# Kernel tuning notes

Measured on AMD Instinct MI355X. Metric: run time of the kernel, lower is better.

## Reference

```python
import jax, jax.numpy as jnp
from jax import lax
import numpy as np

B, T, IN, H, L = 4096, 1024, 2, 16, 3


def _lstm_layer(x_tbd, h0, c0, Wih, Whh, b):
    # x_tbd: [T, B, D_in]; returns hidden states [T, B, H]
    def step(carry, xt):
        h, c = carry
        g = xt @ Wih.T + h @ Whh.T + b  # [B, 4H], gate order i,f,g,o (PyTorch)
        i, f, gg, o = jnp.split(g, 4, axis=-1)
        i = jax.nn.sigmoid(i)
        f = jax.nn.sigmoid(f)
        gg = jnp.tanh(gg)
        o = jax.nn.sigmoid(o)
        c = f * c + i * gg
        h = o * jnp.tanh(c)
        return (h, c), h

    _, hs = lax.scan(step, (h0, c0), x_tbd)
    return hs


def setup_inputs() -> dict:
    key = jax.random.key(0)
    ks = jax.random.split(key, 16)

    def xavier(k, shape):
        fan_out, fan_in = shape
        s = jnp.sqrt(6.0 / (fan_in + fan_out)).astype(jnp.float32)
        return jax.random.uniform(k, shape, jnp.float32, -1.0, 1.0) * s

    inp = {
        "x": jax.random.normal(ks[0], (B, T, IN), jnp.float32),
        "h0": jax.random.normal(ks[1], (L, B, H), jnp.float32) * 0.1,
        "c0": jax.random.normal(ks[2], (L, B, H), jnp.float32) * 0.1,
        "W_ih0": xavier(ks[3], (4 * H, IN)),
        "W_hh0": xavier(ks[4], (4 * H, H)),
        "b_ih0": jnp.zeros((4 * H,), jnp.float32),
        "b_hh0": jnp.zeros((4 * H,), jnp.float32),
        "W_ih1": xavier(ks[5], (4 * H, H)),
        "W_hh1": xavier(ks[6], (4 * H, H)),
        "b_ih1": jnp.zeros((4 * H,), jnp.float32),
        "b_hh1": jnp.zeros((4 * H,), jnp.float32),
        "W_ih2": xavier(ks[7], (4 * H, H)),
        "W_hh2": xavier(ks[8], (4 * H, H)),
        "b_ih2": jnp.zeros((4 * H,), jnp.float32),
        "b_hh2": jnp.zeros((4 * H,), jnp.float32),
        "W_fc": xavier(ks[9], (1, H)),
        "b_fc": jnp.zeros((1,), jnp.float32),
    }
    return inp


def reference(x, h0, c0, W_ih0, W_hh0, b_ih0, b_hh0, W_ih1, W_hh1, b_ih1, b_hh1,
              W_ih2, W_hh2, b_ih2, b_hh2, W_fc, b_fc):
    layers = [
        (W_ih0, W_hh0, b_ih0 + b_hh0),
        (W_ih1, W_hh1, b_ih1 + b_hh1),
        (W_ih2, W_hh2, b_ih2 + b_hh2),
    ]
    h = jnp.transpose(x, (1, 0, 2))  # [T, B, IN]
    for l, (Wih, Whh, b) in enumerate(layers):
        h = _lstm_layer(h, h0[l], c0[l], Wih, Whh, b)  # [T, B, H]
    last = h[-1]  # [B, H] == out[:, -1, :]
    return last @ W_fc.T + b_fc  # [B, 1]
```

## Files before the change

### kernel.cpp

```cpp
#include <hip/hip_runtime.h>

#define NB 4096
#define NT 1024

typedef float f2 __attribute__((ext_vector_type(2)));
typedef float f4 __attribute__((ext_vector_type(4)));

#define GATE(accv, creg, hout) {                                              \
    float e_ = __builtin_amdgcn_exp2f((accv) * kpre);                         \
    float r_ = __builtin_amdgcn_rcpf(1.0f + e_);                              \
    float a_ = fmaf(r_, kA, kB);                                              \
    int ai_ = __float_as_int(a_);                                             \
    float iv_ = __int_as_float(__builtin_amdgcn_mov_dpp(ai_, 0x00, 0xF, 0xF, 0)); \
    float fv_ = __int_as_float(__builtin_amdgcn_mov_dpp(ai_, 0x55, 0xF, 0xF, 0)); \
    float gv_ = __int_as_float(__builtin_amdgcn_mov_dpp(ai_, 0xAA, 0xF, 0xF, 0)); \
    float ov_ = __int_as_float(__builtin_amdgcn_mov_dpp(ai_, 0xFF, 0xF, 0xF, 0)); \
    creg = fmaf(fv_, creg, iv_ * gv_);                                        \
    float e2_ = __builtin_amdgcn_exp2f(creg * -2.88539008177792681f);         \
    float r2_ = __builtin_amdgcn_rcpf(1.0f + e2_);                            \
    hout = ov_ * fmaf(r2_, 2.0f, -1.0f);                                      \
}

__global__ __launch_bounds__(256, 4) void lstm3_kernel(
    const float* __restrict__ x,
    const float* __restrict__ h0,
    const float* __restrict__ c0,
    const float* __restrict__ Wih0, const float* __restrict__ Whh0,
    const float* __restrict__ bih0, const float* __restrict__ bhh0,
    const float* __restrict__ Wih1, const float* __restrict__ Whh1,
    const float* __restrict__ bih1, const float* __restrict__ bhh1,
    const float* __restrict__ Wih2, const float* __restrict__ Whh2,
    const float* __restrict__ bih2, const float* __restrict__ bhh2,
    const float* __restrict__ Wfc,  const float* __restrict__ bfc,
    float* __restrict__ out)
{
    __shared__ float ldsH[3][4][16];
    __shared__ float ldsX[4][64];

    const int lane = threadIdx.x & 63;
    const int wv   = threadIdx.x >> 6;
    const int b    = (blockIdx.x << 2) + wv;
    const int q    = lane >> 2;
    const int g    = lane & 3;
    const int row  = g * 16 + q;

    const float kpre = (g == 2) ? -2.88539008177792681f : -1.44269504088896340f;
    const float kA   = (g == 2) ? 2.0f : 1.0f;
    const float kB   = (g == 2) ? -1.0f : 0.0f;

    f2 wi0 = *(const f2*)&Wih0[row * 2];
    f4 wh0[4], wi1[4], wh1[4], wi2[4], wh2[4];
#pragma unroll
    for (int k = 0; k < 4; ++k) {
        wh0[k] = *(const f4*)&Whh0[row * 16 + 4 * k];
        wi1[k] = *(const f4*)&Wih1[row * 16 + 4 * k];
        wh1[k] = *(const f4*)&Whh1[row * 16 + 4 * k];
        wi2[k] = *(const f4*)&Wih2[row * 16 + 4 * k];
        wh2[k] = *(const f4*)&Whh2[row * 16 + 4 * k];
    }
    float bias0 = bih0[row] + bhh0[row];
    float bias1 = bih1[row] + bhh1[row];
    float bias2 = bih2[row] + bhh2[row];
    asm volatile("" : "+v"(wh0[0]), "+v"(wh0[1]), "+v"(wh0[2]), "+v"(wh0[3]));
    asm volatile("" : "+v"(wi1[0]), "+v"(wi1[1]), "+v"(wi1[2]), "+v"(wi1[3]));
    asm volatile("" : "+v"(wh1[0]), "+v"(wh1[1]), "+v"(wh1[2]), "+v"(wh1[3]));
    asm volatile("" : "+v"(wi2[0]), "+v"(wi2[1]), "+v"(wi2[2]), "+v"(wi2[3]));
    asm volatile("" : "+v"(wh2[0]), "+v"(wh2[1]), "+v"(wh2[2]), "+v"(wh2[3]));
    asm volatile("" : "+v"(wi0), "+v"(bias0), "+v"(bias1), "+v"(bias2));

    float c0r = c0[0 * NB * 16 + b * 16 + q];
    float c1r = c0[1 * NB * 16 + b * 16 + q];
    float c2r = c0[2 * NB * 16 + b * 16 + q];
    if (lane < 16) {
        ldsH[0][wv][lane] = h0[0 * NB * 16 + b * 16 + lane];
        ldsH[1][wv][lane] = h0[1 * NB * 16 + b * 16 + lane];
        ldsH[2][wv][lane] = h0[2 * NB * 16 + b * 16 + lane];
    }
    __builtin_amdgcn_wave_barrier();

    const f4* __restrict__ hb0 = (const f4*)&ldsH[0][wv][0];
    const f4* __restrict__ hb1 = (const f4*)&ldsH[1][wv][0];
    const f4* __restrict__ hb2 = (const f4*)&ldsH[2][wv][0];
    const f2* __restrict__ xb  = (const f2*)&ldsX[wv][0];

    float xpre = x[(size_t)b * (NT * 2) + lane];

    for (int ch = 0; ch < (NT * 2) / 64; ++ch) {
        ldsX[wv][lane] = xpre;
        __builtin_amdgcn_wave_barrier();
        if (ch + 1 < (NT * 2) / 64)
            xpre = x[(size_t)b * (NT * 2) + (ch + 1) * 64 + lane];

#pragma unroll 2
        for (int s = 0; s < 32; ++s) {
            const f2 x2 = xb[s];

            f4 ha = hb0[0], hc = hb0[1], hd = hb0[2], he = hb0[3];
            f4 a0 = wh0[0] * ha;
            f4 a1 = wh0[1] * hc;
            a0 = wh0[2] * hd + a0;
            a1 = wh0[3] * he + a1;
            a0 = a0 + a1;
            f2 s2 = __builtin_shufflevector(a0, a0, 0, 1)
                  + __builtin_shufflevector(a0, a0, 2, 3);
            float acc = (s2.x + s2.y) + fmaf(wi0.x, x2.x, fmaf(wi0.y, x2.y, bias0));
            float hn0;
            GATE(acc, c0r, hn0);
            if (g == 0) ldsH[0][wv][q] = hn0;
            __builtin_amdgcn_wave_barrier();

            ha = hb1[0]; hc = hb1[1]; hd = hb1[2]; he = hb1[3];
            f4 xa = hb0[0], xc = hb0[1], xd = hb0[2], xe = hb0[3];
            a0 = wh1[0] * ha;
            a1 = wh1[1] * hc;
            f4 a2 = wh1[2] * hd;
            f4 a3 = wh1[3] * he;
            a0 = wi1[0] * xa + a0;
            a1 = wi1[1] * xc + a1;
            a2 = wi1[2] * xd + a2;
            a3 = wi1[3] * xe + a3;
            a0 = a0 + a1;
            a2 = a2 + a3;
            a0 = a0 + a2;
            s2 = __builtin_shufflevector(a0, a0, 0, 1)
               + __builtin_shufflevector(a0, a0, 2, 3);
            acc = (s2.x + s2.y) + bias1;
            float hn1;
            GATE(acc, c1r, hn1);
            if (g == 0) ldsH[1][wv][q] = hn1;
            __builtin_amdgcn_wave_barrier();

            ha = hb2[0]; hc = hb2[1]; hd = hb2[2]; he = hb2[3];
            xa = hb1[0]; xc = hb1[1]; xd = hb1[2]; xe = hb1[3];
            a0 = wh2[0] * ha;
            a1 = wh2[1] * hc;
            a2 = wh2[2] * hd;
            a3 = wh2[3] * he;
            a0 = wi2[0] * xa + a0;
            a1 = wi2[1] * xc + a1;
            a2 = wi2[2] * xd + a2;
            a3 = wi2[3] * xe + a3;
            a0 = a0 + a1;
            a2 = a2 + a3;
            a0 = a0 + a2;
            s2 = __builtin_shufflevector(a0, a0, 0, 1)
               + __builtin_shufflevector(a0, a0, 2, 3);
            acc = (s2.x + s2.y) + bias2;
            float hn2;
            GATE(acc, c2r, hn2);
            if (g == 0) ldsH[2][wv][q] = hn2;
            __builtin_amdgcn_wave_barrier();
        }
    }

    if (lane == 0) {
        float s = bfc[0];
#pragma unroll
        for (int k = 0; k < 16; ++k) s = fmaf(ldsH[2][wv][k], Wfc[k], s);
        out[b] = s;
    }
}

extern "C" void kernel_launch(void* const* d_in, const int* in_sizes, int n_in,
                              void* d_out, int out_size, void* d_ws, size_t ws_size,
                              hipStream_t stream) {
    (void)in_sizes; (void)n_in; (void)d_ws; (void)ws_size; (void)out_size;
    const float* x    = (const float*)d_in[0];
    const float* h0   = (const float*)d_in[1];
    const float* c0   = (const float*)d_in[2];
    const float* Wih0 = (const float*)d_in[3];
    const float* Whh0 = (const float*)d_in[4];
    const float* bih0 = (const float*)d_in[5];
    const float* bhh0 = (const float*)d_in[6];
    const float* Wih1 = (const float*)d_in[7];
    const float* Whh1 = (const float*)d_in[8];
    const float* bih1 = (const float*)d_in[9];
    const float* bhh1 = (const float*)d_in[10];
    const float* Wih2 = (const float*)d_in[11];
    const float* Whh2 = (const float*)d_in[12];
    const float* bih2 = (const float*)d_in[13];
    const float* bhh2 = (const float*)d_in[14];
    const float* Wfc  = (const float*)d_in[15];
    const float* bfc  = (const float*)d_in[16];
    float* out = (float*)d_out;

    lstm3_kernel<<<NB / 4, 256, 0, stream>>>(
        x, h0, c0, Wih0, Whh0, bih0, bhh0, Wih1, Whh1, bih1, bhh1,
        Wih2, Whh2, bih2, bhh2, Wfc, bfc, out);
}
```

Measured before the change: 1.169 ms.

## Wavefront-pipeline LSTM layers across three waves per batch element

Each batch element now gets a 192-thread block in which each wave owns one LSTM layer and holds only that layer's weights. The layers run as a skewed wavefront: wave l computes timestep s-l, and hidden states are double-buffered in LDS with a block barrier after every step. This shortens each wave's serial dependency chain to one layer per step and cuts register pressure, in exchange for a __syncthreads per timestep and some idle steps at the start and end of the pipeline.

```diff
diff --git a/kernel.cpp b/kernel.cpp
--- a/kernel.cpp
+++ b/kernel.cpp
@@ -21,7 +21,107 @@
     hout = ov_ * fmaf(r2_, 2.0f, -1.0f);                                      \
 }
 
-__global__ __launch_bounds__(256, 4) void lstm3_kernel(
+#define F2LO(v) __builtin_shufflevector(v, v, 0, 1)
+#define F2HI(v) __builtin_shufflevector(v, v, 2, 3)
+
+#define LOAD_H16(dst, hb) {                                                   \
+    f4 v0_ = *(const f4*)((hb) + 0);                                          \
+    f4 v1_ = *(const f4*)((hb) + 4);                                          \
+    f4 v2_ = *(const f4*)((hb) + 8);                                          \
+    f4 v3_ = *(const f4*)((hb) + 12);                                         \
+    dst[0] = F2LO(v0_); dst[1] = F2HI(v0_);                                   \
+    dst[2] = F2LO(v1_); dst[3] = F2HI(v1_);                                   \
+    dst[4] = F2LO(v2_); dst[5] = F2HI(v2_);                                   \
+    dst[6] = F2LO(v3_); dst[7] = F2HI(v3_);                                   \
+}
+
+#define STEP(S, P, Q)                                                         \
+{                                                                             \
+    if (w == 0) {                                                             \
+        if ((S) < NT) {                                                       \
+            const int t_ = (S);                                               \
+            if ((t_ & 31) == 0) {                                             \
+                X[lane] = xpre;                                               \
+                __builtin_amdgcn_wave_barrier();                              \
+                if (t_ + 32 < NT) { xpre = xg[lane]; xg += 64; }              \
+            }                                                                 \
+            const f2 x2_ = ((const f2*)X)[t_ & 31];                           \
+            f2 hp_[8];                                                        \
+            LOAD_H16(hp_, &H0[Q][0]);                                         \
+            f2 a0_ = wh[0] * hp_[0]; a0_.x += bias;                           \
+            f2 a1_ = wh[1] * hp_[1];                                          \
+            f2 a2_ = wh[2] * hp_[2];                                          \
+            f2 a3_ = wh[3] * hp_[3];                                          \
+            a0_ = wh[4] * hp_[4] + a0_;                                       \
+            a1_ = wh[5] * hp_[5] + a1_;                                       \
+            a2_ = wh[6] * hp_[6] + a2_;                                       \
+            a3_ = wh[7] * hp_[7] + a3_;                                       \
+            a0_ = (a0_ + a1_) + (a2_ + a3_);                                  \
+            float pre_ = a0_.x + a0_.y;                                       \
+            pre_ = fmaf(wix.x, x2_.x, pre_);                                  \
+            pre_ = fmaf(wix.y, x2_.y, pre_);                                  \
+            float hn_;                                                        \
+            GATE(pre_, c, hn_);                                               \
+            H0[P][row] = hn_;                                                 \
+        }                                                                     \
+    } else if (w == 1) {                                                      \
+        if ((S) >= 1 && (S) < NT + 1) {                                       \
+            f2 hp_[8], hi_[8];                                                \
+            LOAD_H16(hi_, &H0[Q][0]);                                         \
+            LOAD_H16(hp_, &H1[P][0]);                                         \
+            f2 a0_ = wh[0] * hp_[0]; a0_.x += bias;                           \
+            f2 a1_ = wh[1] * hp_[1];                                          \
+            f2 a2_ = wh[2] * hp_[2];                                          \
+            f2 a3_ = wh[3] * hp_[3];                                          \
+            a0_ = wh[4] * hp_[4] + a0_;                                       \
+            a1_ = wh[5] * hp_[5] + a1_;                                       \
+            a2_ = wh[6] * hp_[6] + a2_;                                       \
+            a3_ = wh[7] * hp_[7] + a3_;                                       \
+            a0_ = wi[0] * hi_[0] + a0_;                                       \
+            a1_ = wi[1] * hi_[1] + a1_;                                       \
+            a2_ = wi[2] * hi_[2] + a2_;                                       \
+            a3_ = wi[3] * hi_[3] + a3_;                                       \
+            a0_ = wi[4] * hi_[4] + a0_;                                       \
+            a1_ = wi[5] * hi_[5] + a1_;                                       \
+            a2_ = wi[6] * hi_[6] + a2_;                                       \
+            a3_ = wi[7] * hi_[7] + a3_;                                       \
+            a0_ = (a0_ + a1_) + (a2_ + a3_);                                  \
+            float pre_ = a0_.x + a0_.y;                                       \
+            float hn_;                                                        \
+            GATE(pre_, c, hn_);                                               \
+            H1[Q][row] = hn_;                                                 \
+        }                                                                     \
+    } else {                                                                  \
+        if ((S) >= 2) {                                                       \
+            f2 hp_[8], hi_[8];                                                \
+            LOAD_H16(hi_, &H1[P][0]);                                         \
+            LOAD_H16(hp_, &H2[Q][0]);                                         \
+            f2 a0_ = wh[0] * hp_[0]; a0_.x += bias;                           \
+            f2 a1_ = wh[1] * hp_[1];                                          \
+            f2 a2_ = wh[2] * hp_[2];                                          \
+            f2 a3_ = wh[3] * hp_[3];                                          \
+            a0_ = wh[4] * hp_[4] + a0_;                                       \
+            a1_ = wh[5] * hp_[5] + a1_;                                       \
+            a2_ = wh[6] * hp_[6] + a2_;                                       \
+            a3_ = wh[7] * hp_[7] + a3_;                                       \
+            a0_ = wi[0] * hi_[0] + a0_;                                       \
+            a1_ = wi[1] * hi_[1] + a1_;                                       \
+            a2_ = wi[2] * hi_[2] + a2_;                                       \
+            a3_ = wi[3] * hi_[3] + a3_;                                       \
+            a0_ = wi[4] * hi_[4] + a0_;                                       \
+            a1_ = wi[5] * hi_[5] + a1_;                                       \
+            a2_ = wi[6] * hi_[6] + a2_;                                       \
+            a3_ = wi[7] * hi_[7] + a3_;                                       \
+            a0_ = (a0_ + a1_) + (a2_ + a3_);                                  \
+            float pre_ = a0_.x + a0_.y;                                       \
+            float hn_;                                                        \
+            GATE(pre_, c, hn_);                                               \
+            H2[P][row] = hn_;                                                 \
+        }                                                                     \
+    }                                                                         \
+}
+
+__global__ __launch_bounds__(192, 6) void lstm3_kernel(
     const float* __restrict__ x,
     const float* __restrict__ h0,
     const float* __restrict__ c0,
@@ -34,12 +134,12 @@
     const float* __restrict__ Wfc,  const float* __restrict__ bfc,
     float* __restrict__ out)
 {
-    __shared__ float ldsH[3][4][16];
-    __shared__ float ldsX[4][64];
+    __shared__ float H0[2][64], H1[2][64], H2[2][64];
+    __shared__ float X[64];
 
     const int lane = threadIdx.x & 63;
-    const int wv   = threadIdx.x >> 6;
-    const int b    = (blockIdx.x << 2) + wv;
+    const int w    = threadIdx.x >> 6;
+    const int b    = blockIdx.x;
     const int q    = lane >> 2;
     const int g    = lane & 3;
     const int row  = g * 16 + q;
@@ -48,116 +148,72 @@
     const float kA   = (g == 2) ? 2.0f : 1.0f;
     const float kB   = (g == 2) ? -1.0f : 0.0f;
 
-    f2 wi0 = *(const f2*)&Wih0[row * 2];
-    f4 wh0[4], wi1[4], wh1[4], wi2[4], wh2[4];
+    const float* Wihp = (w == 0) ? Wih0 : (w == 1) ? Wih1 : Wih2;
+    const float* Whhp = (w == 0) ? Whh0 : (w == 1) ? Whh1 : Whh2;
+    const float* bihp = (w == 0) ? bih0 : (w == 1) ? bih1 : bih2;
+    const float* bhhp = (w == 0) ? bhh0 : (w == 1) ? bhh1 : bhh2;
+
+    f2 wh[8], wi[8];
+    f2 wix;
 #pragma unroll
     for (int k = 0; k < 4; ++k) {
-        wh0[k] = *(const f4*)&Whh0[row * 16 + 4 * k];
-        wi1[k] = *(const f4*)&Wih1[row * 16 + 4 * k];
-        wh1[k] = *(const f4*)&Whh1[row * 16 + 4 * k];
-        wi2[k] = *(const f4*)&Wih2[row * 16 + 4 * k];
-        wh2[k] = *(const f4*)&Whh2[row * 16 + 4 * k];
-    }
-    float bias0 = bih0[row] + bhh0[row];
-    float bias1 = bih1[row] + bhh1[row];
-    float bias2 = bih2[row] + bhh2[row];
-    asm volatile("" : "+v"(wh0[0]), "+v"(wh0[1]), "+v"(wh0[2]), "+v"(wh0[3]));
-    asm volatile("" : "+v"(wi1[0]), "+v"(wi1[1]), "+v"(wi1[2]), "+v"(wi1[3]));
-    asm volatile("" : "+v"(wh1[0]), "+v"(wh1[1]), "+v"(wh1[2]), "+v"(wh1[3]));
-    asm volatile("" : "+v"(wi2[0]), "+v"(wi2[1]), "+v"(wi2[2]), "+v"(wi2[3]));
-    asm volatile("" : "+v"(wh2[0]), "+v"(wh2[1]), "+v"(wh2[2]), "+v"(wh2[3]));
-    asm volatile("" : "+v"(wi0), "+v"(bias0), "+v"(bias1), "+v"(bias2));
-
-    float c0r = c0[0 * NB * 16 + b * 16 + q];
-    float c1r = c0[1 * NB * 16 + b * 16 + q];
-    float c2r = c0[2 * NB * 16 + b * 16 + q];
-    if (lane < 16) {
-        ldsH[0][wv][lane] = h0[0 * NB * 16 + b * 16 + lane];
-        ldsH[1][wv][lane] = h0[1 * NB * 16 + b * 16 + lane];
-        ldsH[2][wv][lane] = h0[2 * NB * 16 + b * 16 + lane];
-    }
-    __builtin_amdgcn_wave_barrier();
-
-    const f4* __restrict__ hb0 = (const f4*)&ldsH[0][wv][0];
-    const f4* __restrict__ hb1 = (const f4*)&ldsH[1][wv][0];
-    const f4* __restrict__ hb2 = (const f4*)&ldsH[2][wv][0];
-    const f2* __restrict__ xb  = (const f2*)&ldsX[wv][0];
-
-    float xpre = x[(size_t)b * (NT * 2) + lane];
-
-    for (int ch = 0; ch < (NT * 2) / 64; ++ch) {
-        ldsX[wv][lane] = xpre;
-        __builtin_amdgcn_wave_barrier();
-        if (ch + 1 < (NT * 2) / 64)
-            xpre = x[(size_t)b * (NT * 2) + (ch + 1) * 64 + lane];
-
-#pragma unroll 2
-        for (int s = 0; s < 32; ++s) {
-            const f2 x2 = xb[s];
-
-            f4 ha = hb0[0], hc = hb0[1], hd = hb0[2], he = hb0[3];
-            f4 a0 = wh0[0] * ha;
-            f4 a1 = wh0[1] * hc;
-            a0 = wh0[2] * hd + a0;
-            a1 = wh0[3] * he + a1;
-            a0 = a0 + a1;
-            f2 s2 = __builtin_shufflevector(a0, a0, 0, 1)
-                  + __builtin_shufflevector(a0, a0, 2, 3);
-            float acc = (s2.x + s2.y) + fmaf(wi0.x, x2.x, fmaf(wi0.y, x2.y, bias0));
-            float hn0;
-            GATE(acc, c0r, hn0);
-            if (g == 0) ldsH[0][wv][q] = hn0;
-            __builtin_amdgcn_wave_barrier();
-
-            ha = hb1[0]; hc = hb1[1]; hd = hb1[2]; he = hb1[3];
-            f4 xa = hb0[0], xc = hb0[1], xd = hb0[2], xe = hb0[3];
-            a0 = wh1[0] * ha;
-            a1 = wh1[1] * hc;
-            f4 a2 = wh1[2] * hd;
-            f4 a3 = wh1[3] * he;
-            a0 = wi1[0] * xa + a0;
-            a1 = wi1[1] * xc + a1;
-            a2 = wi1[2] * xd + a2;
-            a3 = wi1[3] * xe + a3;
-            a0 = a0 + a1;
-            a2 = a2 + a3;
-            a0 = a0 + a2;
-            s2 = __builtin_shufflevector(a0, a0, 0, 1)
-               + __builtin_shufflevector(a0, a0, 2, 3);
-            acc = (s2.x + s2.y) + bias1;
-            float hn1;
-            GATE(acc, c1r, hn1);
-            if (g == 0) ldsH[1][wv][q] = hn1;
-            __builtin_amdgcn_wave_barrier();
-
-            ha = hb2[0]; hc = hb2[1]; hd = hb2[2]; he = hb2[3];
-            xa = hb1[0]; xc = hb1[1]; xd = hb1[2]; xe = hb1[3];
-            a0 = wh2[0] * ha;
-            a1 = wh2[1] * hc;
-            a2 = wh2[2] * hd;
-            a3 = wh2[3] * he;
-            a0 = wi2[0] * xa + a0;
-            a1 = wi2[1] * xc + a1;
-            a2 = wi2[2] * xd + a2;
-            a3 = wi2[3] * xe + a3;
-            a0 = a0 + a1;
-            a2 = a2 + a3;
-            a0 = a0 + a2;
-            s2 = __builtin_shufflevector(a0, a0, 0, 1)
-               + __builtin_shufflevector(a0, a0, 2, 3);
-            acc = (s2.x + s2.y) + bias2;
-            float hn2;
-            GATE(acc, c2r, hn2);
-            if (g == 0) ldsH[2][wv][q] = hn2;
-            __builtin_amdgcn_wave_barrier();
+        f4 t = *(const f4*)&Whhp[row * 16 + 4 * k];
+        wh[2 * k]     = F2LO(t);
+        wh[2 * k + 1] = F2HI(t);
+    }
+    if (w == 0) {
+        wix = *(const f2*)&Wihp[row * 2];
+    } else {
+#pragma unroll
+        for (int k = 0; k < 4; ++k) {
+            f4 t = *(const f4*)&Wihp[row * 16 + 4 * k];
+            wi[2 * k]     = F2LO(t);
+            wi[2 * k + 1] = F2HI(t);
         }
     }
-
-    if (lane == 0) {
-        float s = bfc[0];
+    const float bias = bihp[row] + bhhp[row];
+
+    float c = c0[w * NB * 16 + b * 16 + q];
+    float* Hown = (w == 0) ? &H0[0][0] : (w == 1) ? &H1[0][0] : &H2[0][0];
+    if (lane < 16)
+        Hown[64 + lane] = h0[w * NB * 16 + b * 16 + lane];
+
+    const float* xg = x + (size_t)b * (NT * 2);
+    float xpre = 0.0f;
+    if (w == 0) { xpre = xg[lane]; xg += 64; }
+
+    __syncthreads();
+
+    int s = 0;
+#pragma unroll 1
+    for (int it = 0; it < (NT + 2) / 2; ++it) {
+        STEP(s, 0, 1);
+        ++s;
+        __syncthreads();
+        STEP(s, 1, 0);
+        ++s;
+        __syncthreads();
+    }
+
+    if (w == 2) {
+        f2 hp[8];
+        LOAD_H16(hp, &H2[1][0]);
+        f2 wf[8];
 #pragma unroll
-        for (int k = 0; k < 16; ++k) s = fmaf(ldsH[2][wv][k], Wfc[k], s);
-        out[b] = s;
+        for (int k = 0; k < 4; ++k) {
+            f4 t = *(const f4*)&Wfc[4 * k];
+            wf[2 * k]     = F2LO(t);
+            wf[2 * k + 1] = F2HI(t);
+        }
+        f2 a0 = wf[0] * hp[0] + wf[1] * hp[1];
+        f2 a1 = wf[2] * hp[2] + wf[3] * hp[3];
+        a0 = wf[4] * hp[4] + a0;
+        a1 = wf[5] * hp[5] + a1;
+        a0 = wf[6] * hp[6] + a0;
+        a1 = wf[7] * hp[7] + a1;
+        a0 = a0 + a1;
+        if (lane == 0)
+            out[b] = a0.x + a0.y + bfc[0];
     }
 }
 
@@ -184,7 +240,7 @@
     const float* bfc  = (const float*)d_in[16];
     float* out = (float*)d_out;
 
-    lstm3_kernel<<<NB / 4, 256, 0, stream>>>(
+    lstm3_kernel<<<NB, 192, 0, stream>>>(
         x, h0, c0, Wih0, Whh0, bih0, bhh0, Wih1, Whh1, bih1, bhh1,
         Wih2, Whh2, bih2, bhh2, Wfc, bfc, out);
 }
```

New measurement: 1.060 ms. 1.1x faster.
